# Performance work log

Hardware: AMD Instinct MI355X
Metric: run time of the kernel (lower is better)

## Reference

```python
import jax, jax.numpy as jnp
import numpy as np
from jax import lax

B, C_IN, C_OUT, K, N_W, L = 32, 256, 256, 7, 8, 4096
SQ = C_IN // 32  # squeezed dim = 8
STRIDE, PAD = 1, 3


def setup_inputs() -> dict:
    key = jax.random.key(0)
    ks = jax.random.split(key, 8)
    s = 0.05
    return {
        "x": jax.random.normal(ks[0], (B, C_IN, L), dtype=jnp.float32),
        "conv_weight": jax.random.normal(ks[1], (C_OUT, C_IN, K, N_W), dtype=jnp.float32) * s,
        "w1": jax.random.normal(ks[2], (C_IN, SQ), dtype=jnp.float32) * s,   # linear1 weight (x @ w1)
        "b1": jax.random.normal(ks[3], (SQ,), dtype=jnp.float32) * s,
        "wk": jax.random.normal(ks[4], (SQ, K), dtype=jnp.float32) * s,      # kernel head
        "wi": jax.random.normal(ks[5], (SQ, C_IN), dtype=jnp.float32) * s,   # inc head
        "wo": jax.random.normal(ks[6], (SQ, C_OUT), dtype=jnp.float32) * s,  # outc head
        "wn": jax.random.normal(ks[7], (SQ, N_W), dtype=jnp.float32) * s,    # nums head
    }


def reference(x, conv_weight, w1, b1, wk, wi, wo, wn):
    # SqueezeFeedForward: AdaptiveAvgPool1d(1) == mean over length, then Linear + exact GELU
    pooled = jnp.mean(x, axis=-1)                        # [B, C_in]
    h = jax.nn.gelu(pooled @ w1 + b1, approximate=False)  # [B, SQ]

    kr = jax.nn.sigmoid(h @ wk)          # [B, K]
    inc = jax.nn.sigmoid(h @ wi)         # [B, C_in]
    outc = jax.nn.sigmoid(h @ wo)        # [B, C_out]
    nums = jax.nn.softmax(h @ wn, -1)    # [B, N_w]

    # Per-sample mixed weights: sum over num_weight of 4-way outer-product gated base weight
    w = jnp.einsum('bk,bi,bo,bn,oikn->boik', kr, inc, outc, nums, conv_weight)  # [B,O,I,K]

    b, o, i, k = w.shape
    l = x.shape[-1]
    # Batched per-sample conv via grouped conv: groups = B
    lhs = x.reshape(1, b * i, l)         # [1, B*I, L]
    rhs = w.reshape(b * o, i, k)         # [B*O, I, K]
    out = lax.conv_general_dilated(
        lhs, rhs,
        window_strides=(STRIDE,),
        padding=[(PAD, PAD)],
        dimension_numbers=('NCH', 'OIH', 'NCH'),
        feature_group_count=b,
    )
    return out.reshape(b, o, -1)         # [B, O, L_out]
```

## Files before the change

### kernel.cpp

```cpp
#include <hip/hip_runtime.h>
#include <hip/hip_bf16.h>
#include <math.h>

#define B_   32
#define CI   256
#define CO   256
#define KW   7
#define NW   8
#define SQD  8
#define L_   4096

typedef __attribute__((ext_vector_type(8))) __bf16 bf16x8;
typedef __attribute__((ext_vector_type(4))) float  f32x4;

static __device__ __forceinline__ unsigned short f2bf(float f) {
    unsigned int u = __builtin_bit_cast(unsigned int, f);
    u += 0x7FFFu + ((u >> 16) & 1u);
    return (unsigned short)(u >> 16);
}

__global__ __launch_bounds__(256) void k1_mean_transpose(
        const float* __restrict__ x,
        unsigned short* __restrict__ xT,
        float* __restrict__ pooled) {
    int b  = blockIdx.z;
    int i0 = blockIdx.y * 64;
    int l0 = blockIdx.x * 128;
    __shared__ float tile[64][129];
    int t  = threadIdx.x;
    int lv = (t & 31) * 4;
    int ib = t >> 5;

    const float* xb = x + (size_t)b * CI * L_;
    for (int it = 0; it < 8; ++it) {
        int i = ib + 8 * it;
        float4 v = *(const float4*)(xb + (size_t)(i0 + i) * L_ + l0 + lv);
        tile[i][lv + 0] = v.x;
        tile[i][lv + 1] = v.y;
        tile[i][lv + 2] = v.z;
        tile[i][lv + 3] = v.w;
        float ps = v.x + v.y + v.z + v.w;
        for (int m = 1; m <= 16; m <<= 1) ps += __shfl_xor(ps, m);
        if ((t & 31) == 0) atomicAdd(pooled + b * CI + i0 + i, ps);
    }
    __syncthreads();
    for (int u = t; u < 128 * 8; u += 256) {
        int l = u >> 3, ig = u & 7;
        unsigned int pk[4];
#pragma unroll
        for (int q = 0; q < 4; ++q) {
            float a = tile[ig * 8 + 2 * q + 0][l];
            float c = tile[ig * 8 + 2 * q + 1][l];
            pk[q] = (unsigned int)f2bf(a) | ((unsigned int)f2bf(c) << 16);
        }
        uint4 w4; w4.x = pk[0]; w4.y = pk[1]; w4.z = pk[2]; w4.w = pk[3];
        *(uint4*)(xT + ((size_t)b * L_ + l0 + l) * CI + i0 + ig * 8) = w4;
    }
}

__global__ __launch_bounds__(64) void k2_gates(
        const float* __restrict__ pooled,
        const float* __restrict__ w1, const float* __restrict__ b1,
        const float* __restrict__ wk, const float* __restrict__ wi,
        const float* __restrict__ wo, const float* __restrict__ wn,
        float* __restrict__ kr,
        float* __restrict__ inc,
        float* __restrict__ outc,
        float* __restrict__ nums)
{
    int b = blockIdx.x, lane = threadIdx.x;
    float pc[4];
#pragma unroll
    for (int j = 0; j < 4; ++j)
        pc[j] = pooled[b * CI + lane + 64 * j] * (1.0f / L_);
    float h[SQD];
#pragma unroll
    for (int s = 0; s < SQD; ++s) {
        float ps = 0.f;
#pragma unroll
        for (int j = 0; j < 4; ++j)
            ps += pc[j] * w1[(lane + 64 * j) * SQD + s];
        for (int m = 1; m <= 32; m <<= 1) ps += __shfl_xor(ps, m);
        float z = ps + b1[s];
        h[s] = 0.5f * z * (1.0f + erff(z * 0.70710678118654752f));
    }
    if (lane < KW) {
        float a = 0.f;
#pragma unroll
        for (int s = 0; s < SQD; ++s) a += h[s] * wk[s * KW + lane];
        kr[b * 8 + lane] = 1.0f / (1.0f + expf(-a));
    }
    if (lane < NW) {
        float e[NW]; float mx = -1e30f;
#pragma unroll
        for (int n = 0; n < NW; ++n) {
            float a = 0.f;
#pragma unroll
            for (int s = 0; s < SQD; ++s) a += h[s] * wn[s * NW + n];
            e[n] = a; mx = fmaxf(mx, a);
        }
        float den = 0.f;
#pragma unroll
        for (int n = 0; n < NW; ++n) den += expf(e[n] - mx);
        nums[b * NW + lane] = expf(e[lane] - mx) / den;
    }
#pragma unroll
    for (int j = 0; j < 4; ++j) {
        int c = lane + 64 * j;
        float a = 0.f, o2 = 0.f;
#pragma unroll
        for (int s = 0; s < SQD; ++s) {
            a  += h[s] * wi[s * CI + c];
            o2 += h[s] * wo[s * CO + c];
        }
        inc[b * CI + c]  = 1.0f / (1.0f + expf(-a));
        outc[b * CO + c] = 1.0f / (1.0f + expf(-o2));
    }
}

__global__ __launch_bounds__(256) void k3_wgen(
        const float* __restrict__ cw,
        const float* __restrict__ kr, const float* __restrict__ inc,
        const float* __restrict__ outc, const float* __restrict__ nums,
        unsigned short* __restrict__ W2) {
    __shared__ float s_nums[B_][NW];
    __shared__ float s_kr[B_][KW];
    __shared__ float s_inc[B_][32];
    __shared__ float s_outc[B_][8];
    int t = threadIdx.x;
    int ic = blockIdx.x & 7, o0 = (blockIdx.x >> 3) * 8;
    s_nums[t >> 3][t & 7] = nums[t];
    if (t < B_ * KW) s_kr[t / KW][t % KW] = kr[(t / KW) * 8 + (t % KW)];
    for (int u = t; u < 32 * 32; u += 256) {
        int bb = u >> 5, ii = u & 31;
        s_inc[bb][ii] = inc[bb * CI + ic * 32 + ii];
    }
    for (int u = t; u < 32 * 8; u += 256) {
        int bb = u >> 3, oo = u & 7;
        s_outc[bb][oo] = outc[bb * CO + o0 + oo];
    }
    __syncthreads();
    int ii = t & 31, oo = t >> 5;
    int o = o0 + oo, i = ic * 32 + ii;
    float cwv[KW][NW];
    const float* p = cw + ((size_t)(o * CI + i)) * (KW * NW);
#pragma unroll
    for (int k = 0; k < KW; ++k)
#pragma unroll
        for (int n = 0; n < NW; ++n) cwv[k][n] = p[k * NW + n];
    for (int bb = 0; bb < B_; ++bb) {
        float gio = s_inc[bb][ii] * s_outc[bb][oo];
#pragma unroll
        for (int k = 0; k < KW; ++k) {
            float sk = 0.f;
#pragma unroll
            for (int n = 0; n < NW; ++n) sk += s_nums[bb][n] * cwv[k][n];
            float w = s_kr[bb][k] * gio * sk;
            W2[(((size_t)(bb * KW + k) * 8 + ic) * CO + o) * 32 + ii] = f2bf(w);
        }
    }
}

__global__ __launch_bounds__(512, 2) void k4_conv(
        const unsigned short* __restrict__ xT,
        const unsigned short* __restrict__ W2,
        float* __restrict__ out) {
    __shared__ __align__(16) unsigned short xs[262 * 256];
    int b = blockIdx.y, l0 = blockIdx.x * 256;
    int t = threadIdx.x;

    for (int u = t; u < 262 * 32; u += 512) {
        int r = u >> 5, c = u & 31;
        int gl = l0 - 3 + r;
        uint4 v = make_uint4(0u, 0u, 0u, 0u);
        if (gl >= 0 && gl < L_)
            v = *(const uint4*)(xT + ((size_t)b * L_ + gl) * CI + c * 8);
        *(uint4*)(xs + r * 256 + (c ^ (r & 7)) * 8) = v;
    }
    __syncthreads();

    int lane = t & 63, wid = t >> 6;
    int o_base = (wid & 3) * 64;
    int l_off  = (wid >> 2) * 128;
    int ml = lane & 15, kg = lane >> 4;

    f32x4 acc[4][8];
#pragma unroll
    for (int a = 0; a < 4; ++a)
#pragma unroll
        for (int c = 0; c < 8; ++c) acc[a][c] = (f32x4){0.f, 0.f, 0.f, 0.f};

    const unsigned short* wbase = W2 + (size_t)b * (KW * 8 * CO * 32);
    for (int k = 0; k < KW; ++k) {
        const unsigned short* wk_ = wbase + (size_t)k * (8 * CO * 32);
#pragma unroll
        for (int icc = 0; icc < 8; ++icc) {
            const unsigned short* wkc = wk_ + icc * (CO * 32);
            bf16x8 af[4];
#pragma unroll
            for (int mt = 0; mt < 4; ++mt)
                af[mt] = *(const bf16x8*)(wkc + (o_base + mt * 16 + ml) * 32 + kg * 8);
            bf16x8 bfr[8];
#pragma unroll
            for (int nt = 0; nt < 8; ++nt) {
                int r = l_off + nt * 16 + ml + k;
                int unit = (icc * 4 + kg) ^ (r & 7);
                bfr[nt] = *(const bf16x8*)(xs + r * 256 + unit * 8);
            }
#pragma unroll
            for (int mt = 0; mt < 4; ++mt)
#pragma unroll
                for (int nt = 0; nt < 8; ++nt)
                    acc[mt][nt] = __builtin_amdgcn_mfma_f32_16x16x32_bf16(
                        af[mt], bfr[nt], acc[mt][nt], 0, 0, 0);
        }
    }

#pragma unroll
    for (int mt = 0; mt < 4; ++mt) {
        int o = o_base + mt * 16 + kg * 4;
#pragma unroll
        for (int nt = 0; nt < 8; ++nt) {
            int l = l0 + l_off + nt * 16 + ml;
            float* po = out + ((size_t)(b * CO + o)) * L_ + l;
#pragma unroll
            for (int q = 0; q < 4; ++q)
                po[(size_t)q * L_] = acc[mt][nt][q];
        }
    }
}

extern "C" void kernel_launch(void* const* d_in, const int* in_sizes, int n_in,
                              void* d_out, int out_size, void* d_ws, size_t ws_size,
                              hipStream_t stream) {
    const float* x  = (const float*)d_in[0];
    const float* cw = (const float*)d_in[1];
    const float* w1 = (const float*)d_in[2];
    const float* b1 = (const float*)d_in[3];
    const float* wk = (const float*)d_in[4];
    const float* wi = (const float*)d_in[5];
    const float* wo = (const float*)d_in[6];
    const float* wn = (const float*)d_in[7];
    float* out = (float*)d_out;

    char* ws = (char*)d_ws;
    const size_t off_xT     = 0;
    const size_t off_W2     = 67108864;
    const size_t off_pooled = 96468992;
    const size_t off_kr     = 96501760;
    const size_t off_inc    = 96502784;
    const size_t off_outc   = 96535552;
    const size_t off_nums   = 96568320;

    unsigned short* xT  = (unsigned short*)(ws + off_xT);
    unsigned short* W2  = (unsigned short*)(ws + off_W2);
    float* pooled = (float*)(ws + off_pooled);
    float* kr     = (float*)(ws + off_kr);
    float* inc    = (float*)(ws + off_inc);
    float* outc   = (float*)(ws + off_outc);
    float* nums   = (float*)(ws + off_nums);

    hipMemsetAsync(pooled, 0, B_ * CI * sizeof(float), stream);
    k1_mean_transpose<<<dim3(32, 4, B_), 256, 0, stream>>>(x, xT, pooled);
    k2_gates<<<B_, 64, 0, stream>>>(pooled, w1, b1, wk, wi, wo, wn,
                                    kr, inc, outc, nums);
    k3_wgen<<<256, 256, 0, stream>>>(cw, kr, inc, outc, nums, W2);
    k4_conv<<<dim3(16, 32), 512, 0, stream>>>(xT, W2, out);
}
```

Measured before the change: 201.4 us.

## Fuse x transpose/bf16 conversion into conv kernel and shrink conv tiles

Removes the separate transposed bf16 copy of x: k1 now only computes per-row means, and the conv kernel loads fp32 x directly, converts to bf16 and writes it into swizzled shared memory, including halo rows. The conv tile shrinks from 256 to 128 positions per block with each wave owning 32 output channels, which cuts LDS use and allows 4 blocks per CU. Block IDs are remapped so that neighbouring blocks spread across batches, and s_setprio is placed around the MFMA bursts. This saves the 64MB xT write and read-back, but the conv kernel now performs strided scalar LDS stores and reloads each x halo per block.

```diff
diff --git a/kernel.cpp b/kernel.cpp
--- a/kernel.cpp
+++ b/kernel.cpp
@@ -19,43 +19,23 @@
     return (unsigned short)(u >> 16);
 }
 
-__global__ __launch_bounds__(256) void k1_mean_transpose(
-        const float* __restrict__ x,
-        unsigned short* __restrict__ xT,
-        float* __restrict__ pooled) {
-    int b  = blockIdx.z;
-    int i0 = blockIdx.y * 64;
-    int l0 = blockIdx.x * 128;
-    __shared__ float tile[64][129];
-    int t  = threadIdx.x;
-    int lv = (t & 31) * 4;
-    int ib = t >> 5;
-
-    const float* xb = x + (size_t)b * CI * L_;
-    for (int it = 0; it < 8; ++it) {
-        int i = ib + 8 * it;
-        float4 v = *(const float4*)(xb + (size_t)(i0 + i) * L_ + l0 + lv);
-        tile[i][lv + 0] = v.x;
-        tile[i][lv + 1] = v.y;
-        tile[i][lv + 2] = v.z;
-        tile[i][lv + 3] = v.w;
-        float ps = v.x + v.y + v.z + v.w;
-        for (int m = 1; m <= 16; m <<= 1) ps += __shfl_xor(ps, m);
-        if ((t & 31) == 0) atomicAdd(pooled + b * CI + i0 + i, ps);
-    }
+__global__ __launch_bounds__(256) void k1_mean(
+        const float* __restrict__ x, float* __restrict__ pooled) {
+    int row = blockIdx.x;
+    const float* p = x + (size_t)row * L_;
+    int t = threadIdx.x;
+    float s = 0.f;
+#pragma unroll
+    for (int it = 0; it < 4; ++it) {
+        float4 v = *(const float4*)(p + (size_t)(t + 256 * it) * 4);
+        s += v.x + v.y + v.z + v.w;
+    }
+    for (int m = 1; m <= 32; m <<= 1) s += __shfl_xor(s, m);
+    __shared__ float wsum[4];
+    if ((t & 63) == 0) wsum[t >> 6] = s;
     __syncthreads();
-    for (int u = t; u < 128 * 8; u += 256) {
-        int l = u >> 3, ig = u & 7;
-        unsigned int pk[4];
-#pragma unroll
-        for (int q = 0; q < 4; ++q) {
-            float a = tile[ig * 8 + 2 * q + 0][l];
-            float c = tile[ig * 8 + 2 * q + 1][l];
-            pk[q] = (unsigned int)f2bf(a) | ((unsigned int)f2bf(c) << 16);
-        }
-        uint4 w4; w4.x = pk[0]; w4.y = pk[1]; w4.z = pk[2]; w4.w = pk[3];
-        *(uint4*)(xT + ((size_t)b * L_ + l0 + l) * CI + i0 + ig * 8) = w4;
-    }
+    if (t == 0)
+        pooled[row] = (wsum[0] + wsum[1] + wsum[2] + wsum[3]) * (1.0f / L_);
 }
 
 __global__ __launch_bounds__(64) void k2_gates(
@@ -72,7 +52,7 @@
     float pc[4];
 #pragma unroll
     for (int j = 0; j < 4; ++j)
-        pc[j] = pooled[b * CI + lane + 64 * j] * (1.0f / L_);
+        pc[j] = pooled[b * CI + lane + 64 * j];
     float h[SQD];
 #pragma unroll
     for (int s = 0; s < SQD; ++s) {
@@ -161,32 +141,47 @@
     }
 }
 
-__global__ __launch_bounds__(512, 2) void k4_conv(
-        const unsigned short* __restrict__ xT,
+__global__ __launch_bounds__(512, 4) void k4_conv(
+        const float* __restrict__ x,
         const unsigned short* __restrict__ W2,
         float* __restrict__ out) {
-    __shared__ __align__(16) unsigned short xs[262 * 256];
-    int b = blockIdx.y, l0 = blockIdx.x * 256;
+    __shared__ __align__(16) unsigned short xs[134 * 256];
+    int bid = blockIdx.x;
+    int wg  = (bid & 7) * 128 + (bid >> 3);
+    int b = wg >> 5, l0 = (wg & 31) * 128;
     int t = threadIdx.x;
-
-    for (int u = t; u < 262 * 32; u += 512) {
-        int r = u >> 5, c = u & 31;
+    const float* xb = x + (size_t)b * CI * L_;
+
+    {
+        int c = t & 31;
+        int i = t >> 5;
+#pragma unroll 4
+        for (int it = 0; it < 16; ++it, i += 16) {
+            float4 v = *(const float4*)(xb + (size_t)i * L_ + l0 + c * 4);
+            int u0 = i >> 3, isub = i & 7;
+#pragma unroll
+            for (int j = 0; j < 4; ++j) {
+                int r = c * 4 + j + 3;
+                xs[r * 256 + ((u0 ^ (r & 7)) * 8) + isub] = f2bf((&v.x)[j]);
+            }
+        }
+    }
+    for (int u = t; u < 6 * 256; u += 512) {
+        int h = u >> 8, i = u & 255;
+        int r = (h < 3) ? h : 128 + h;
         int gl = l0 - 3 + r;
-        uint4 v = make_uint4(0u, 0u, 0u, 0u);
-        if (gl >= 0 && gl < L_)
-            v = *(const uint4*)(xT + ((size_t)b * L_ + gl) * CI + c * 8);
-        *(uint4*)(xs + r * 256 + (c ^ (r & 7)) * 8) = v;
+        float f = (gl >= 0 && gl < L_) ? xb[(size_t)i * L_ + gl] : 0.f;
+        xs[r * 256 + (((i >> 3) ^ (r & 7)) * 8) + (i & 7)] = f2bf(f);
     }
     __syncthreads();
 
     int lane = t & 63, wid = t >> 6;
-    int o_base = (wid & 3) * 64;
-    int l_off  = (wid >> 2) * 128;
+    int o_base = wid * 32;
     int ml = lane & 15, kg = lane >> 4;
 
-    f32x4 acc[4][8];
-#pragma unroll
-    for (int a = 0; a < 4; ++a)
+    f32x4 acc[2][8];
+#pragma unroll
+    for (int a = 0; a < 2; ++a)
 #pragma unroll
         for (int c = 0; c < 8; ++c) acc[a][c] = (f32x4){0.f, 0.f, 0.f, 0.f};
 
@@ -196,32 +191,34 @@
 #pragma unroll
         for (int icc = 0; icc < 8; ++icc) {
             const unsigned short* wkc = wk_ + icc * (CO * 32);
-            bf16x8 af[4];
-#pragma unroll
-            for (int mt = 0; mt < 4; ++mt)
+            bf16x8 af[2];
+#pragma unroll
+            for (int mt = 0; mt < 2; ++mt)
                 af[mt] = *(const bf16x8*)(wkc + (o_base + mt * 16 + ml) * 32 + kg * 8);
             bf16x8 bfr[8];
 #pragma unroll
             for (int nt = 0; nt < 8; ++nt) {
-                int r = l_off + nt * 16 + ml + k;
+                int r = nt * 16 + ml + k;
                 int unit = (icc * 4 + kg) ^ (r & 7);
                 bfr[nt] = *(const bf16x8*)(xs + r * 256 + unit * 8);
             }
-#pragma unroll
-            for (int mt = 0; mt < 4; ++mt)
+            __builtin_amdgcn_s_setprio(1);
+#pragma unroll
+            for (int mt = 0; mt < 2; ++mt)
 #pragma unroll
                 for (int nt = 0; nt < 8; ++nt)
                     acc[mt][nt] = __builtin_amdgcn_mfma_f32_16x16x32_bf16(
                         af[mt], bfr[nt], acc[mt][nt], 0, 0, 0);
-        }
-    }
-
-#pragma unroll
-    for (int mt = 0; mt < 4; ++mt) {
+            __builtin_amdgcn_s_setprio(0);
+        }
+    }
+
+#pragma unroll
+    for (int mt = 0; mt < 2; ++mt) {
         int o = o_base + mt * 16 + kg * 4;
 #pragma unroll
         for (int nt = 0; nt < 8; ++nt) {
-            int l = l0 + l_off + nt * 16 + ml;
+            int l = l0 + nt * 16 + ml;
             float* po = out + ((size_t)(b * CO + o)) * L_ + l;
 #pragma unroll
             for (int q = 0; q < 4; ++q)
@@ -244,26 +241,23 @@
     float* out = (float*)d_out;
 
     char* ws = (char*)d_ws;
-    const size_t off_xT     = 0;
-    const size_t off_W2     = 67108864;
-    const size_t off_pooled = 96468992;
-    const size_t off_kr     = 96501760;
-    const size_t off_inc    = 96502784;
-    const size_t off_outc   = 96535552;
-    const size_t off_nums   = 96568320;
-
-    unsigned short* xT  = (unsigned short*)(ws + off_xT);
-    unsigned short* W2  = (unsigned short*)(ws + off_W2);
+    const size_t off_W2     = 0;
+    const size_t off_pooled = 29360128;
+    const size_t off_kr     = 29392896;
+    const size_t off_inc    = 29393920;
+    const size_t off_outc   = 29426688;
+    const size_t off_nums   = 29459456;
+
+    unsigned short* W2 = (unsigned short*)(ws + off_W2);
     float* pooled = (float*)(ws + off_pooled);
     float* kr     = (float*)(ws + off_kr);
     float* inc    = (float*)(ws + off_inc);
     float* outc   = (float*)(ws + off_outc);
     float* nums   = (float*)(ws + off_nums);
 
-    hipMemsetAsync(pooled, 0, B_ * CI * sizeof(float), stream);
-    k1_mean_transpose<<<dim3(32, 4, B_), 256, 0, stream>>>(x, xT, pooled);
+    k1_mean<<<B_ * CI, 256, 0, stream>>>(x, pooled);
     k2_gates<<<B_, 64, 0, stream>>>(pooled, w1, b1, wk, wi, wo, wn,
                                     kr, inc, outc, nums);
     k3_wgen<<<256, 256, 0, stream>>>(cw, kr, inc, outc, nums, W2);
-    k4_conv<<<dim3(16, 32), 512, 0, stream>>>(xT, W2, out);
-}
+    k4_conv<<<1024, 512, 0, stream>>>(x, W2, out);
+}
```

After: 175.4 us. 12.9% less time.
